# Kernel optimization log

Hardware: AMD Instinct MI355X
Metric: run time of the kernel (lower is better)

Reference implementation:

```python
import jax, jax.numpy as jnp
import numpy as np

E = 16          # num_experts
D_FULL = 1024   # full_feature_dim
DM = 128        # expert_dim
S = D_FULL // E # per-expert feature slice = 64
P = 2048        # num patches
B = 8
C = 256
W = 3           # local_window (neighbor experts)
DEPTH = 8       # cantor_depth
NEG = -1e9


def _cantor_coord(pos, max_len, depth):
    x = pos / max(1, max_len - 1)
    x = max(1e-6, min(x, 1.0 - 1e-6))
    val, factor = 0.0, 0.5
    for _ in range(depth):
        x *= 3.0
        d = int(x)
        x -= d
        if d == 2:
            val += factor
        factor *= 0.5
    return val


def _expert_routes():
    coords = np.array([_cantor_coord(i, E, DEPTH) for i in range(E)], dtype=np.float32)
    return np.stack([np.argsort(np.abs(coords - coords[i]), kind='stable')[:W] for i in range(E)]).astype(np.int32)


ROUTES = _expert_routes()  # [E, W] static routing table


def setup_inputs():
    key = jax.random.key(0)
    ks = jax.random.split(key, 8)
    h = S // 4
    lim = float(np.sqrt(6.0 / (S + DM)))  # xavier_uniform bound
    penta = jax.random.normal(ks[5], (E, 5, DM), jnp.float32) * 0.02
    penta = penta / jnp.linalg.norm(penta, axis=-1, keepdims=True)
    return {
        'tokens': jax.random.normal(ks[0], (B, P, D_FULL), jnp.float32),
        'fingerprints': jax.random.uniform(ks[1], (P,), jnp.float32),
        'alpha': jnp.ones((E,), jnp.float32),
        'gate_w1': jax.random.normal(ks[2], (E, S, h), jnp.float32) * 0.05,
        'gate_b1': jnp.zeros((E, h), jnp.float32),
        'gate_w2': jax.random.normal(ks[3], (E, h, 1), jnp.float32) * 0.05,
        'gate_b2': jnp.zeros((E, 1), jnp.float32),
        'q_w': jax.random.uniform(ks[4], (E, S, DM), jnp.float32, -lim, lim),
        'k_w': jax.random.uniform(ks[6], (E, S, DM), jnp.float32, -lim, lim),
        'v_w': jax.random.uniform(ks[7], (E, S, DM), jnp.float32, -lim, lim),
        'penta': penta,
        'fusion_w': jnp.ones((5,), jnp.float32) / 5.0,
        'temperature': jnp.float32(0.5),
    }


def _dispatch(fingerprints):
    # Fingerprint band masks, then fixed-capacity gather (static shapes for jit).
    masks = []
    for e in range(E):
        lo, hi = e / E, (e + 1) / E
        m = (fingerprints >= lo) & ((fingerprints <= hi) if e == E - 1 else (fingerprints < hi))
        masks.append(m)
    masks = jnp.stack(masks)                             # [E, P]
    order = jnp.argsort(jnp.where(masks, 0, 1), axis=1)  # stable: assigned patches first
    idx = order[:, :C]                                   # [E, C]
    valid = jnp.take_along_axis(masks, idx, axis=1)      # [E, C]
    return idx, valid


def _forward(tokens, fingerprints, alpha, gate_w1, gate_b1, gate_w2, gate_b2,
             q_w, k_w, v_w, penta, fusion_w, temperature):
    idx, valid = _dispatch(fingerprints)
    Kaff, Qaff, Vs = [], [], []
    for e in range(E):  # fixed structural loop over experts
        feats = tokens[:, idx[e], e * S:(e + 1) * S]                       # [B, C, S]
        g = jax.nn.sigmoid(jax.nn.gelu(feats @ gate_w1[e] + gate_b1[e]) @ gate_w2[e] + gate_b2[e])
        aw = jax.nn.sigmoid(alpha[e])
        feats = feats * (g * aw + (1.0 - aw))                              # gated features
        Q = feats @ q_w[e]
        K = feats @ k_w[e]
        V = feats @ v_w[e]                                                 # [B, C, DM]
        dirs = penta[e] / jnp.linalg.norm(penta[e], axis=-1, keepdims=True)  # [5, DM]
        Kaff.append(jnp.einsum('bcd,vd->vbc', K, dirs))
        Qaff.append(jnp.einsum('bcd,vd->vbc', Q, dirs))
        Vs.append(V)
    Kaff = jnp.stack(Kaff)   # [E, 5, B, C]
    Qaff = jnp.stack(Qaff)   # [E, 5, B, C]
    Vs = jnp.stack(Vs)       # [E, B, C, DM]
    wdir = jax.nn.softmax(fusion_w)
    vmask = valid.astype(jnp.float32)
    out = jnp.zeros((B, P, DM), jnp.float32)
    for e in range(E):
        nb = ROUTES[e]                                  # static [W]
        Knb, Vnb, vnb = Kaff[nb], Vs[nb], vmask[nb]     # [W,5,B,C], [W,B,C,DM], [W,C]
        scores = jnp.einsum('vbi,nvbj->vbinj', Qaff[e], Knb) / temperature
        scores = jnp.where(vnb[None, None, None, :, :] > 0, scores, NEG)
        attn = jax.nn.softmax(scores.reshape(5, B, C, W * C), axis=-1).reshape(5, B, C, W, C)
        att = jnp.einsum('vbinj,nbjd->vbid', attn, Vnb)  # per-direction attended values
        out_e = jnp.einsum('v,vbid->bid', wdir, att) * vmask[e][None, :, None]
        out = out.at[:, idx[e]].add(out_e)              # scatter back to patch positions
    return out


def reference(tokens, fingerprints, alpha, gate_w1, gate_b1, gate_w2, gate_b2,
              q_w, k_w, v_w, penta, fusion_w, temperature):
    return _forward(tokens, fingerprints, alpha, gate_w1, gate_b1, gate_w2, gate_b2,
                    q_w, k_w, v_w, penta, fusion_w, temperature)
```

## Files before the change

kernel.cpp:

```cpp
#include <hip/hip_runtime.h>
#include <cfloat>
#include <math.h>

#define E 16
#define DFULL 1024
#define DM 128
#define S 64
#define P 2048
#define B 8
#define C 256
#define W 3
#define H 16
#define RQ 16
#define NCH 16
#define LOG2E 1.4426950408889634f

typedef __attribute__((ext_vector_type(8))) short short8;
typedef __attribute__((ext_vector_type(4))) float f32x4;
#define MFMA_BF16(a, b, c) __builtin_amdgcn_mfma_f32_16x16x32_bf16((a), (b), (c), 0, 0, 0)

struct RoutesArg { int nb[E][W]; };

static void compute_routes(int r[E][W]) {
  float coords[E];
  for (int i = 0; i < E; ++i) {
    double x = (double)i / (double)(E - 1);
    if (x < 1e-06) x = 1e-06;
    if (x > 1.0 - 1e-06) x = 1.0 - 1e-06;
    double val = 0.0, factor = 0.5;
    for (int k = 0; k < 8; ++k) {
      x *= 3.0;
      int d = (int)x;
      x -= (double)d;
      if (d == 2) val += factor;
      factor *= 0.5;
    }
    coords[i] = (float)val;
  }
  for (int e = 0; e < E; ++e) {
    float de[E];
    for (int i = 0; i < E; ++i) de[i] = fabsf(coords[i] - coords[e]);
    bool used[E] = {false};
    for (int w = 0; w < W; ++w) {
      int best = -1; float bd = FLT_MAX;
      for (int i = 0; i < E; ++i)
        if (!used[i] && de[i] < bd) { bd = de[i]; best = i; }
      used[best] = true;
      r[e][w] = best;
    }
  }
}

__device__ __forceinline__ unsigned short bfhi(float x) {
  return (unsigned short)(__float_as_uint(x) >> 16);
}
__device__ __forceinline__ float bf2f(unsigned short h) {
  return __uint_as_float(((unsigned)h) << 16);
}
__device__ __forceinline__ float gelu_tanh(float x) {
  float x3 = x * x * x;
  return 0.5f * x * (1.0f + tanhf(0.7978845608028654f * (x + 0.044715f * x3)));
}
__device__ __forceinline__ float sigmoidf_(float x) {
  return 1.0f / (1.0f + __expf(-x));
}

__global__ __launch_bounds__(256) void k_setup(
    const float* __restrict__ fp, const float* __restrict__ qw,
    const float* __restrict__ kw, const float* __restrict__ penta,
    const float* __restrict__ temp, const float* __restrict__ vw,
    int* __restrict__ idx, int* __restrict__ counts,
    unsigned short* __restrict__ qkdT_h, unsigned short* __restrict__ qkdT_l,
    unsigned short* __restrict__ vwT_h, unsigned short* __restrict__ vwT_l) {
  int e = blockIdx.x, t = threadIdx.x;
  if (blockIdx.y == 1) {
    const float* vwe = vw + (size_t)e * S * DM;
    for (int u = t; u < S * DM; u += 256) {
      int d = u >> 6, s = u & 63;
      float f = vwe[(size_t)s * DM + d];
      unsigned short h = bfhi(f), l = bfhi(f - bf2f(h));
      vwT_h[(size_t)e * 8192 + u] = h;
      vwT_l[(size_t)e * 8192 + u] = l;
    }
    return;
  }
  {
    float lo = (float)e * 0.0625f, hi = (float)(e + 1) * 0.0625f;
    bool last = (e == E - 1);
    int p0 = t * 8;
    int m[8]; int ls = 0;
    #pragma unroll
    for (int k = 0; k < 8; ++k) {
      float f = fp[p0 + k];
      bool mm = (f >= lo) && (last ? (f <= hi) : (f < hi));
      m[k] = mm ? 1 : 0;
      ls += m[k];
    }
    __shared__ int sc[256];
    sc[t] = ls;
    __syncthreads();
    for (int o = 1; o < 256; o <<= 1) {
      int v = (t >= o) ? sc[t - o] : 0;
      __syncthreads();
      sc[t] += v;
      __syncthreads();
    }
    int incl = sc[t];
    int M = sc[255];
    int r = incl - ls;
    #pragma unroll
    for (int k = 0; k < 8; ++k) {
      if (m[k]) {
        if (r < C) idx[e * C + r] = p0 + k;
        r++;
      }
    }
    if (t == 0) counts[e] = (M < C) ? M : C;
  }
  __syncthreads();
  __shared__ float s_rn[5];
  if (t < 5) {
    const float* pv = penta + (e * 5 + t) * DM;
    float ss = 0.f;
    for (int d = 0; d < DM; ++d) ss += pv[d] * pv[d];
    s_rn[t] = 1.0f / sqrtf(ss);
  }
  __syncthreads();
  float invT = 1.0f / temp[0];
  int s = t & 63, cg = t >> 6;
  for (int c = cg; c < 10; c += 4) {
    int v = c % 5;
    bool isq = (c < 5);
    const float* wrow = (isq ? qw : kw) + ((size_t)e * S + s) * DM;
    const float* pv = penta + (e * 5 + v) * DM;
    float acc = 0.f;
    #pragma unroll
    for (int d4 = 0; d4 < DM / 4; ++d4) {
      float4 a = ((const float4*)wrow)[d4];
      float4 p = ((const float4*)pv)[d4];
      acc += a.x * p.x + a.y * p.y + a.z * p.z + a.w * p.w;
    }
    float val = acc * s_rn[v] * (isq ? invT : 1.0f);
    unsigned short h = bfhi(val), l = bfhi(val - bf2f(h));
    qkdT_h[(e * 16 + c) * 64 + s] = h;
    qkdT_l[(e * 16 + c) * 64 + s] = l;
  }
  for (int c = 10 + cg; c < 16; c += 4) {
    qkdT_h[(e * 16 + c) * 64 + s] = 0;
    qkdT_l[(e * 16 + c) * 64 + s] = 0;
  }
}

__global__ __launch_bounds__(256) void k_p1(
    const float* __restrict__ tokens, const float* __restrict__ alpha,
    const float* __restrict__ gw1, const float* __restrict__ gb1,
    const float* __restrict__ gw2, const float* __restrict__ gb2,
    const unsigned short* __restrict__ qkdT_h, const unsigned short* __restrict__ qkdT_l,
    const unsigned short* __restrict__ vwT_h, const unsigned short* __restrict__ vwT_l,
    const int* __restrict__ idx, const int* __restrict__ counts,
    float* __restrict__ Qa, float* __restrict__ Ka,
    unsigned short* __restrict__ Vt_h, unsigned short* __restrict__ Vt_l,
    float* __restrict__ kmx, float* __restrict__ kmn) {
  int e = blockIdx.x, b = blockIdx.y, rq = blockIdx.z;
  int t = threadIdx.x;
  int Me = counts[e];
  int r0 = rq * RQ;

  if (r0 >= Me) {
    if (t < 5) {
      kmx[((e * 5 + t) * B + b) * NCH + rq] = -FLT_MAX;
      kmn[((e * 5 + t) * B + b) * NCH + rq] = FLT_MAX;
    }
    return;
  }

  __shared__ float s_f[RQ * 65];
  __shared__ __align__(16) unsigned short s_fh[RQ * 72];
  __shared__ __align__(16) unsigned short s_fl[RQ * 72];
  __shared__ float s_gw1[S * H];
  __shared__ float s_gh[RQ * 8 * H];
  __shared__ float s_scl[RQ];
  __shared__ float s_kx[5 * RQ], s_kn[5 * RQ];
  __shared__ __align__(16) unsigned short s_vth[DM * 16];
  __shared__ __align__(16) unsigned short s_vtl[DM * 16];

  {
    int row = t >> 4, q4 = t & 15;
    int ii = r0 + row;
    int pos = (ii < Me) ? idx[e * C + ii] : idx[e * C];
    const float* trow = tokens + ((size_t)b * P + pos) * DFULL + e * S;
    float4 v4 = ((const float4*)trow)[q4];
    s_f[row * 65 + q4 * 4 + 0] = v4.x;
    s_f[row * 65 + q4 * 4 + 1] = v4.y;
    s_f[row * 65 + q4 * 4 + 2] = v4.z;
    s_f[row * 65 + q4 * 4 + 3] = v4.w;
    ((float4*)s_gw1)[t] = ((const float4*)(gw1 + (size_t)e * S * H))[t];
  }
  __syncthreads();

  if (t < 128) {
    int row = t >> 3, sq = t & 7;
    float hh[H];
    #pragma unroll
    for (int j = 0; j < H; ++j) hh[j] = 0.f;
    #pragma unroll
    for (int k = 0; k < 8; ++k) {
      int s = sq * 8 + k;
      float fs = s_f[row * 65 + s];
      const float* gr = s_gw1 + s * H;
      #pragma unroll
      for (int j = 0; j < H; ++j) hh[j] += fs * gr[j];
    }
    #pragma unroll
    for (int j = 0; j < H; ++j) s_gh[(row * 8 + sq) * H + j] = hh[j];
  }
  __syncthreads();
  if (t < RQ) {
    float z = gb2[e];
    #pragma unroll
    for (int j = 0; j < H; ++j) {
      float hj = gb1[e * H + j];
      #pragma unroll
      for (int p = 0; p < 8; ++p) hj += s_gh[(t * 8 + p) * H + j];
      z += gelu_tanh(hj) * gw2[e * H + j];
    }
    float aw = sigmoidf_(alpha[e]);
    s_scl[t] = sigmoidf_(z) * aw + (1.0f - aw);
  }
  __syncthreads();
  {
    int row = t >> 4, s0 = (t & 15) * 4;
    float sc = s_scl[row];
    #pragma unroll
    for (int k = 0; k < 4; ++k) {
      float f = s_f[row * 65 + s0 + k] * sc;
      unsigned short h = bfhi(f), l = bfhi(f - bf2f(h));
      s_fh[row * 72 + s0 + k] = h;
      s_fl[row * 72 + s0 + k] = l;
    }
  }
  __syncthreads();

  int L = t & 63, wv = t >> 6, quad = L >> 4, col = L & 15;

  {
    const unsigned short* vTh = vwT_h + (size_t)e * 8192;
    const unsigned short* vTl = vwT_l + (size_t)e * 8192;
    f32x4 va0 = {0.f, 0.f, 0.f, 0.f}, va1 = {0.f, 0.f, 0.f, 0.f};
    int d0 = wv * 32 + col, d1 = d0 + 16;
    #pragma unroll
    for (int kc = 0; kc < 2; ++kc) {
      int ko = kc * 32 + quad * 8;
      short8 ah = *(const short8*)(s_fh + col * 72 + ko);
      short8 al = *(const short8*)(s_fl + col * 72 + ko);
      short8 bh0 = *(const short8*)(vTh + d0 * 64 + ko);
      short8 bl0 = *(const short8*)(vTl + d0 * 64 + ko);
      short8 bh1 = *(const short8*)(vTh + d1 * 64 + ko);
      short8 bl1 = *(const short8*)(vTl + d1 * 64 + ko);
      va0 = MFMA_BF16(ah, bh0, va0);
      va0 = MFMA_BF16(ah, bl0, va0);
      va0 = MFMA_BF16(al, bh0, va0);
      va1 = MFMA_BF16(ah, bh1, va1);
      va1 = MFMA_BF16(ah, bl1, va1);
      va1 = MFMA_BF16(al, bh1, va1);
    }
    #pragma unroll
    for (int reg = 0; reg < 4; ++reg) {
      int row = quad * 4 + reg;
      float f0 = va0[reg];
      unsigned short h0 = bfhi(f0), l0 = bfhi(f0 - bf2f(h0));
      s_vth[d0 * 16 + row] = h0;
      s_vtl[d0 * 16 + row] = l0;
      float f1 = va1[reg];
      unsigned short h1 = bfhi(f1), l1 = bfhi(f1 - bf2f(h1));
      s_vth[d1 * 16 + row] = h1;
      s_vtl[d1 * 16 + row] = l1;
    }
  }

  if (wv == 0) {
    const unsigned short* qTh = qkdT_h + e * 16 * 64;
    const unsigned short* qTl = qkdT_l + e * 16 * 64;
    f32x4 qa = {0.f, 0.f, 0.f, 0.f};
    #pragma unroll
    for (int kc = 0; kc < 2; ++kc) {
      int ko = kc * 32 + quad * 8;
      short8 ah = *(const short8*)(s_fh + col * 72 + ko);
      short8 al = *(const short8*)(s_fl + col * 72 + ko);
      short8 bh = *(const short8*)(qTh + col * 64 + ko);
      short8 bl = *(const short8*)(qTl + col * 64 + ko);
      qa = MFMA_BF16(ah, bh, qa);
      qa = MFMA_BF16(ah, bl, qa);
      qa = MFMA_BF16(al, bh, qa);
    }
    #pragma unroll
    for (int reg = 0; reg < 4; ++reg) {
      int row = quad * 4 + reg;
      int ii = r0 + row;
      float val = qa[reg];
      if (col < 5) {
        if (ii < Me) Qa[((e * 5 + col) * B + b) * C + ii] = val;
      } else if (col < 10) {
        int v = col - 5;
        if (ii < Me) Ka[((e * 5 + v) * B + b) * C + ii] = val;
        s_kx[v * RQ + row] = (ii < Me) ? val : -FLT_MAX;
        s_kn[v * RQ + row] = (ii < Me) ? val : FLT_MAX;
      }
    }
  }
  __syncthreads();
  if (t < 5) {
    float mx = -FLT_MAX, mn = FLT_MAX;
    for (int r = 0; r < RQ; ++r) {
      mx = fmaxf(mx, s_kx[t * RQ + r]);
      mn = fminf(mn, s_kn[t * RQ + r]);
    }
    kmx[((e * 5 + t) * B + b) * NCH + rq] = mx;
    kmn[((e * 5 + t) * B + b) * NCH + rq] = mn;
  }
  {
    size_t base = ((size_t)(e * B + b) * 16 + rq) * (DM * 16);
    int off = t * 8;
    *(short8*)(Vt_h + base + off) = *(const short8*)(s_vth + off);
    *(short8*)(Vt_l + base + off) = *(const short8*)(s_vtl + off);
  }
}

__global__ __launch_bounds__(256) void k_p2v(
    const float* __restrict__ Qa, const float* __restrict__ Ka,
    const unsigned short* __restrict__ Vt_h, const unsigned short* __restrict__ Vt_l,
    const float* __restrict__ kmx, const float* __restrict__ kmn,
    const int* __restrict__ idx, const int* __restrict__ counts,
    const float* __restrict__ fusw, float* __restrict__ out, RoutesArg R) {
  int e = blockIdx.x, b = blockIdx.y, rq = blockIdx.z;
  int t = threadIdx.x;
  int Me = counts[e];
  int r0 = rq * RQ;
  if (r0 >= Me) return;

  __shared__ float s_ka[3 * 5 * C];
  __shared__ __align__(16) unsigned short s_wh[RQ * 264];
  __shared__ __align__(16) unsigned short s_wl[RQ * 264];
  __shared__ float s_lp[16 * 5 * RQ];
  __shared__ float s_KX[5], s_KN[5];
  __shared__ float s_l[5 * RQ];
  float* s_red = (float*)s_wh;

  int nbs[3] = {R.nb[e][0], R.nb[e][1], R.nb[e][2]};
  int Mns[3] = {counts[nbs[0]], counts[nbs[1]], counts[nbs[2]]};
  int row = t & 15, jq = t >> 4;
  int ii = r0 + row;

  for (int u = t; u < 3 * 5 * C; u += 256) {
    int n = u / (5 * C);
    int rem = u - n * 5 * C;
    int v = rem >> 8, j = rem & 255;
    s_ka[u] = Ka[(((size_t)nbs[n] * 5 + v) * B + b) * C + j];
  }
  if (t < 240) {
    int v = t / 48, rr = t % 48, n = rr >> 4, k = rr & 15;
    int base = ((nbs[n] * 5 + v) * B + b) * NCH + k;
    s_red[t] = kmx[base];
    s_red[240 + t] = kmn[base];
  }
  __syncthreads();
  if (t < 5) {
    float KX = -FLT_MAX, KN = FLT_MAX;
    for (int u = 0; u < 48; ++u) {
      KX = fmaxf(KX, s_red[t * 48 + u]);
      KN = fminf(KN, s_red[240 + t * 48 + u]);
    }
    s_KX[t] = KX; s_KN[t] = KN;
  }
  __syncthreads();

  float q2[5], m2[5];
  #pragma unroll
  for (int v = 0; v < 5; ++v) {
    float qv = Qa[(((size_t)e * 5 + v) * B + b) * C + ii];
    q2[v] = qv * LOG2E;
    m2[v] = ((qv > 0.f) ? qv * s_KX[v] : qv * s_KN[v]) * LOG2E;
  }

  float lp[5] = {0.f, 0.f, 0.f, 0.f, 0.f};
  for (int n = 0; n < 3; ++n) {
    int Mn = Mns[n];
    const float* kb = s_ka + n * 5 * C;
    for (int j = jq; j < Mn; j += 16) {
      #pragma unroll
      for (int v = 0; v < 5; ++v)
        lp[v] += exp2f(fmaf(q2[v], kb[v * C + j], -m2[v]));
    }
  }
  #pragma unroll
  for (int v = 0; v < 5; ++v) s_lp[(jq * 5 + v) * RQ + row] = lp[v];
  __syncthreads();
  if (t < 80) {
    int v = t >> 4, rw = t & 15;
    float l = 0.f;
    #pragma unroll
    for (int g = 0; g < 16; ++g) l += s_lp[(g * 5 + v) * RQ + rw];
    s_l[v * RQ + rw] = l;
  }
  __syncthreads();

  float fw[5];
  #pragma unroll
  for (int v = 0; v < 5; ++v) fw[v] = fusw[v];
  float fmx = fw[0];
  #pragma unroll
  for (int v = 1; v < 5; ++v) fmx = fmaxf(fmx, fw[v]);
  float fsum = 0.f;
  #pragma unroll
  for (int v = 0; v < 5; ++v) { fw[v] = __expf(fw[v] - fmx); fsum += fw[v]; }
  float c2[5];
  #pragma unroll
  for (int v = 0; v < 5; ++v) {
    float cl = (fw[v] / fsum) / s_l[v * RQ + row];
    c2[v] = __log2f(cl) - m2[v];
  }

  int L = t & 63, wv = t >> 6, quad = L >> 4, col = L & 15;
  int d0 = wv * 32 + col, d1 = d0 + 16;
  f32x4 acc0 = {0.f, 0.f, 0.f, 0.f}, acc1 = {0.f, 0.f, 0.f, 0.f};

  for (int n = 0; n < 3; ++n) {
    int ne = nbs[n], Mn = Mns[n];
    const float* kb = s_ka + n * 5 * C;
    __syncthreads();
    #pragma unroll
    for (int h8 = 0; h8 < 2; ++h8) {
      short8 wh8, wl8;
      #pragma unroll
      for (int k2 = 0; k2 < 8; ++k2) {
        int jj = jq * 16 + h8 * 8 + k2;
        float ww = 0.f;
        if (jj < Mn) {
          #pragma unroll
          for (int v = 0; v < 5; ++v)
            ww += exp2f(fmaf(q2[v], kb[v * C + jj], c2[v]));
        }
        unsigned short h = bfhi(ww), l = bfhi(ww - bf2f(h));
        wh8[k2] = (short)h;
        wl8[k2] = (short)l;
      }
      *(short8*)(s_wh + row * 264 + jq * 16 + h8 * 8) = wh8;
      *(short8*)(s_wl + row * 264 + jq * 16 + h8 * 8) = wl8;
    }
    __syncthreads();
    const unsigned short* vbh = Vt_h + (size_t)(ne * B + b) * (DM * C);
    const unsigned short* vbl = Vt_l + (size_t)(ne * B + b) * (DM * C);
    int kcN = (Mn + 31) >> 5;
    for (int kc = 0; kc < kcN; ++kc) {
      int ko = kc * 32 + quad * 8;
      short8 ah = *(const short8*)(s_wh + col * 264 + ko);
      short8 al = *(const short8*)(s_wl + col * 264 + ko);
      int jt = kc * 2 + (quad >> 1);
      size_t sb = (size_t)jt * (DM * 16) + (quad & 1) * 8;
      short8 bh0 = *(const short8*)(vbh + sb + d0 * 16);
      short8 bl0 = *(const short8*)(vbl + sb + d0 * 16);
      short8 bh1 = *(const short8*)(vbh + sb + d1 * 16);
      short8 bl1 = *(const short8*)(vbl + sb + d1 * 16);
      acc0 = MFMA_BF16(ah, bh0, acc0);
      acc0 = MFMA_BF16(ah, bl0, acc0);
      acc0 = MFMA_BF16(al, bh0, acc0);
      acc1 = MFMA_BF16(ah, bh1, acc1);
      acc1 = MFMA_BF16(ah, bl1, acc1);
      acc1 = MFMA_BF16(al, bh1, acc1);
    }
  }

  #pragma unroll
  for (int reg = 0; reg < 4; ++reg) {
    int rr = quad * 4 + reg;
    int iw = r0 + rr;
    if (iw < Me) {
      int pos = idx[e * C + iw];
      float* orow = out + ((size_t)b * P + pos) * DM;
      orow[d0] = acc0[reg];
      orow[d1] = acc1[reg];
    }
  }
}

extern "C" void kernel_launch(void* const* d_in, const int* in_sizes, int n_in,
                              void* d_out, int out_size, void* d_ws, size_t ws_size,
                              hipStream_t stream) {
  const float* tokens = (const float*)d_in[0];
  const float* fingerprints = (const float*)d_in[1];
  const float* alpha = (const float*)d_in[2];
  const float* gw1 = (const float*)d_in[3];
  const float* gb1 = (const float*)d_in[4];
  const float* gw2 = (const float*)d_in[5];
  const float* gb2 = (const float*)d_in[6];
  const float* qw = (const float*)d_in[7];
  const float* kw = (const float*)d_in[8];
  const float* vw = (const float*)d_in[9];
  const float* penta = (const float*)d_in[10];
  const float* fusw = (const float*)d_in[11];
  const float* temp = (const float*)d_in[12];
  float* out = (float*)d_out;

  float* ws = (float*)d_ws;
  float* Qa = ws;
  float* Ka = Qa + (size_t)E * 5 * B * C;
  float* kmx = Ka + (size_t)E * 5 * B * C;
  float* kmn = kmx + (size_t)E * 5 * B * NCH;
  unsigned short* qkdT_h = (unsigned short*)(kmn + (size_t)E * 5 * B * NCH);
  unsigned short* qkdT_l = qkdT_h + (size_t)E * 16 * 64;
  unsigned short* vwT_h = qkdT_l + (size_t)E * 16 * 64;
  unsigned short* vwT_l = vwT_h + (size_t)E * S * DM;
  unsigned short* Vt_h = vwT_l + (size_t)E * S * DM;
  unsigned short* Vt_l = Vt_h + (size_t)E * B * DM * C;
  int* idx = (int*)(Vt_l + (size_t)E * B * DM * C);
  int* counts = idx + (size_t)E * C;

  RoutesArg R;
  compute_routes(R.nb);

  hipMemsetAsync(d_out, 0, (size_t)out_size * sizeof(float), stream);
  k_setup<<<dim3(E, 2), dim3(256), 0, stream>>>(fingerprints, qw, kw, penta, temp, vw,
                                                idx, counts, qkdT_h, qkdT_l, vwT_h, vwT_l);
  k_p1<<<dim3(E, B, NCH), dim3(256), 0, stream>>>(tokens, alpha, gw1, gb1, gw2, gb2,
                                                  qkdT_h, qkdT_l, vwT_h, vwT_l,
                                                  idx, counts, Qa, Ka, Vt_h, Vt_l,
                                                  kmx, kmn);
  k_p2v<<<dim3(E, B, NCH), dim3(256), 0, stream>>>(Qa, Ka, Vt_h, Vt_l, kmx, kmn,
                                                   idx, counts, fusw, out, R);
}
```

Baseline: 209.0 us.

## Double threads per block, fuse output zeroing, restage neighbor keys and V layout

Launches k_p1 and k_p2v with 512 threads so each wave computes one 16-column slice of the MFMA output instead of two. It drops the separate memset and has k_p1 blocks zero the output. k_p2v now stages one neighbor's keys at a time in shared memory instead of all three, and V is stored in a layout that gives contiguous 8-element loads. k_setup transposes v_w through shared memory for coalesced reads. Together these aim at more parallelism and lower LDS use, at the cost of extra syncs per neighbor.

Result: faster. 190.7 us (-8.7%).

```diff
diff --git a/kernel.cpp b/kernel.cpp
--- a/kernel.cpp
+++ b/kernel.cpp
@@ -14,6 +14,7 @@
 #define RQ 16
 #define NCH 16
 #define LOG2E 1.4426950408889634f
+#define WST 272
 
 typedef __attribute__((ext_vector_type(8))) short short8;
 typedef __attribute__((ext_vector_type(4))) float f32x4;
@@ -73,11 +74,17 @@
     unsigned short* __restrict__ qkdT_h, unsigned short* __restrict__ qkdT_l,
     unsigned short* __restrict__ vwT_h, unsigned short* __restrict__ vwT_l) {
   int e = blockIdx.x, t = threadIdx.x;
+  __shared__ float s_tr[DM * 65];
   if (blockIdx.y == 1) {
     const float* vwe = vw + (size_t)e * S * DM;
     for (int u = t; u < S * DM; u += 256) {
+      int s = u >> 7, d = u & 127;
+      s_tr[d * 65 + s] = vwe[u];
+    }
+    __syncthreads();
+    for (int u = t; u < S * DM; u += 256) {
       int d = u >> 6, s = u & 63;
-      float f = vwe[(size_t)s * DM + d];
+      float f = s_tr[d * 65 + s];
       unsigned short h = bfhi(f), l = bfhi(f - bf2f(h));
       vwT_h[(size_t)e * 8192 + u] = h;
       vwT_l[(size_t)e * 8192 + u] = l;
@@ -151,7 +158,7 @@
   }
 }
 
-__global__ __launch_bounds__(256) void k_p1(
+__global__ __launch_bounds__(512, 8) void k_p1(
     const float* __restrict__ tokens, const float* __restrict__ alpha,
     const float* __restrict__ gw1, const float* __restrict__ gb1,
     const float* __restrict__ gw2, const float* __restrict__ gb2,
@@ -160,12 +167,21 @@
     const int* __restrict__ idx, const int* __restrict__ counts,
     float* __restrict__ Qa, float* __restrict__ Ka,
     unsigned short* __restrict__ Vt_h, unsigned short* __restrict__ Vt_l,
-    float* __restrict__ kmx, float* __restrict__ kmn) {
+    float* __restrict__ kmx, float* __restrict__ kmn,
+    float* __restrict__ out) {
   int e = blockIdx.x, b = blockIdx.y, rq = blockIdx.z;
   int t = threadIdx.x;
+
+  {
+    int blk = (e * B + b) * NCH + rq;
+    if (t < 256) {
+      float4 z4 = {0.f, 0.f, 0.f, 0.f};
+      ((float4*)out)[(size_t)blk * 256 + t] = z4;
+    }
+  }
+
   int Me = counts[e];
   int r0 = rq * RQ;
-
   if (r0 >= Me) {
     if (t < 5) {
       kmx[((e * 5 + t) * B + b) * NCH + rq] = -FLT_MAX;
@@ -184,7 +200,7 @@
   __shared__ __align__(16) unsigned short s_vth[DM * 16];
   __shared__ __align__(16) unsigned short s_vtl[DM * 16];
 
-  {
+  if (t < 256) {
     int row = t >> 4, q4 = t & 15;
     int ii = r0 + row;
     int pos = (ii < Me) ? idx[e * C + ii] : idx[e * C];
@@ -228,7 +244,7 @@
     s_scl[t] = sigmoidf_(z) * aw + (1.0f - aw);
   }
   __syncthreads();
-  {
+  if (t < 256) {
     int row = t >> 4, s0 = (t & 15) * 4;
     float sc = s_scl[row];
     #pragma unroll
@@ -246,35 +262,26 @@
   {
     const unsigned short* vTh = vwT_h + (size_t)e * 8192;
     const unsigned short* vTl = vwT_l + (size_t)e * 8192;
-    f32x4 va0 = {0.f, 0.f, 0.f, 0.f}, va1 = {0.f, 0.f, 0.f, 0.f};
-    int d0 = wv * 32 + col, d1 = d0 + 16;
+    f32x4 va = {0.f, 0.f, 0.f, 0.f};
+    int d0 = wv * 16 + col;
     #pragma unroll
     for (int kc = 0; kc < 2; ++kc) {
       int ko = kc * 32 + quad * 8;
       short8 ah = *(const short8*)(s_fh + col * 72 + ko);
       short8 al = *(const short8*)(s_fl + col * 72 + ko);
-      short8 bh0 = *(const short8*)(vTh + d0 * 64 + ko);
-      short8 bl0 = *(const short8*)(vTl + d0 * 64 + ko);
-      short8 bh1 = *(const short8*)(vTh + d1 * 64 + ko);
-      short8 bl1 = *(const short8*)(vTl + d1 * 64 + ko);
-      va0 = MFMA_BF16(ah, bh0, va0);
-      va0 = MFMA_BF16(ah, bl0, va0);
-      va0 = MFMA_BF16(al, bh0, va0);
-      va1 = MFMA_BF16(ah, bh1, va1);
-      va1 = MFMA_BF16(ah, bl1, va1);
-      va1 = MFMA_BF16(al, bh1, va1);
+      short8 bh = *(const short8*)(vTh + d0 * 64 + ko);
+      short8 bl = *(const short8*)(vTl + d0 * 64 + ko);
+      va = MFMA_BF16(ah, bh, va);
+      va = MFMA_BF16(ah, bl, va);
+      va = MFMA_BF16(al, bh, va);
     }
     #pragma unroll
     for (int reg = 0; reg < 4; ++reg) {
       int row = quad * 4 + reg;
-      float f0 = va0[reg];
+      float f0 = va[reg];
       unsigned short h0 = bfhi(f0), l0 = bfhi(f0 - bf2f(h0));
       s_vth[d0 * 16 + row] = h0;
       s_vtl[d0 * 16 + row] = l0;
-      float f1 = va1[reg];
-      unsigned short h1 = bfhi(f1), l1 = bfhi(f1 - bf2f(h1));
-      s_vth[d1 * 16 + row] = h1;
-      s_vtl[d1 * 16 + row] = l1;
     }
   }
 
@@ -318,15 +325,17 @@
     kmx[((e * 5 + t) * B + b) * NCH + rq] = mx;
     kmn[((e * 5 + t) * B + b) * NCH + rq] = mn;
   }
-  {
-    size_t base = ((size_t)(e * B + b) * 16 + rq) * (DM * 16);
-    int off = t * 8;
-    *(short8*)(Vt_h + base + off) = *(const short8*)(s_vth + off);
-    *(short8*)(Vt_l + base + off) = *(const short8*)(s_vtl + off);
-  }
-}
-
-__global__ __launch_bounds__(256) void k_p2v(
+  if (t < 256) {
+    size_t base = (size_t)(e * B + b) * (DM * C);
+    int jsl = t >> 7, d = t & 127;
+    size_t dst = base + ((size_t)(rq * 2 + jsl) * DM + d) * 8;
+    int src = d * 16 + jsl * 8;
+    *(short8*)(Vt_h + dst) = *(const short8*)(s_vth + src);
+    *(short8*)(Vt_l + dst) = *(const short8*)(s_vtl + src);
+  }
+}
+
+__global__ __launch_bounds__(512, 8) void k_p2v(
     const float* __restrict__ Qa, const float* __restrict__ Ka,
     const unsigned short* __restrict__ Vt_h, const unsigned short* __restrict__ Vt_l,
     const float* __restrict__ kmx, const float* __restrict__ kmn,
@@ -338,10 +347,10 @@
   int r0 = rq * RQ;
   if (r0 >= Me) return;
 
-  __shared__ float s_ka[3 * 5 * C];
-  __shared__ __align__(16) unsigned short s_wh[RQ * 264];
-  __shared__ __align__(16) unsigned short s_wl[RQ * 264];
-  __shared__ float s_lp[16 * 5 * RQ];
+  __shared__ float s_ka[5 * C];
+  __shared__ __align__(16) unsigned short s_wh[RQ * WST];
+  __shared__ __align__(16) unsigned short s_wl[RQ * WST];
+  __shared__ float s_lp[32 * 5 * RQ];
   __shared__ float s_KX[5], s_KN[5];
   __shared__ float s_l[5 * RQ];
   float* s_red = (float*)s_wh;
@@ -351,12 +360,6 @@
   int row = t & 15, jq = t >> 4;
   int ii = r0 + row;
 
-  for (int u = t; u < 3 * 5 * C; u += 256) {
-    int n = u / (5 * C);
-    int rem = u - n * 5 * C;
-    int v = rem >> 8, j = rem & 255;
-    s_ka[u] = Ka[(((size_t)nbs[n] * 5 + v) * B + b) * C + j];
-  }
   if (t < 240) {
     int v = t / 48, rr = t % 48, n = rr >> 4, k = rr & 15;
     int base = ((nbs[n] * 5 + v) * B + b) * NCH + k;
@@ -384,12 +387,18 @@
 
   float lp[5] = {0.f, 0.f, 0.f, 0.f, 0.f};
   for (int n = 0; n < 3; ++n) {
+    __syncthreads();
+    if (t < 320) {
+      int v = t >> 6, off = t & 63;
+      ((float4*)s_ka)[v * 64 + off] =
+          ((const float4*)(Ka + (((size_t)nbs[n] * 5 + v) * B + b) * C))[off];
+    }
+    __syncthreads();
     int Mn = Mns[n];
-    const float* kb = s_ka + n * 5 * C;
-    for (int j = jq; j < Mn; j += 16) {
+    for (int j = jq; j < Mn; j += 32) {
       #pragma unroll
       for (int v = 0; v < 5; ++v)
-        lp[v] += exp2f(fmaf(q2[v], kb[v * C + j], -m2[v]));
+        lp[v] += exp2f(fmaf(q2[v], s_ka[v * C + j], -m2[v]));
     }
   }
   #pragma unroll
@@ -399,7 +408,7 @@
     int v = t >> 4, rw = t & 15;
     float l = 0.f;
     #pragma unroll
-    for (int g = 0; g < 16; ++g) l += s_lp[(g * 5 + v) * RQ + rw];
+    for (int g = 0; g < 32; ++g) l += s_lp[(g * 5 + v) * RQ + rw];
     s_l[v * RQ + rw] = l;
   }
   __syncthreads();
@@ -421,31 +430,35 @@
   }
 
   int L = t & 63, wv = t >> 6, quad = L >> 4, col = L & 15;
-  int d0 = wv * 32 + col, d1 = d0 + 16;
-  f32x4 acc0 = {0.f, 0.f, 0.f, 0.f}, acc1 = {0.f, 0.f, 0.f, 0.f};
+  int d0 = wv * 16 + col;
+  f32x4 acc = {0.f, 0.f, 0.f, 0.f};
 
   for (int n = 0; n < 3; ++n) {
     int ne = nbs[n], Mn = Mns[n];
-    const float* kb = s_ka + n * 5 * C;
-    __syncthreads();
-    #pragma unroll
-    for (int h8 = 0; h8 < 2; ++h8) {
+    __syncthreads();
+    if (t < 320) {
+      int v = t >> 6, off = t & 63;
+      ((float4*)s_ka)[v * 64 + off] =
+          ((const float4*)(Ka + (((size_t)ne * 5 + v) * B + b) * C))[off];
+    }
+    __syncthreads();
+    {
       short8 wh8, wl8;
       #pragma unroll
       for (int k2 = 0; k2 < 8; ++k2) {
-        int jj = jq * 16 + h8 * 8 + k2;
+        int jj = jq * 8 + k2;
         float ww = 0.f;
         if (jj < Mn) {
           #pragma unroll
           for (int v = 0; v < 5; ++v)
-            ww += exp2f(fmaf(q2[v], kb[v * C + jj], c2[v]));
+            ww += exp2f(fmaf(q2[v], s_ka[v * C + jj], c2[v]));
         }
         unsigned short h = bfhi(ww), l = bfhi(ww - bf2f(h));
         wh8[k2] = (short)h;
         wl8[k2] = (short)l;
       }
-      *(short8*)(s_wh + row * 264 + jq * 16 + h8 * 8) = wh8;
-      *(short8*)(s_wl + row * 264 + jq * 16 + h8 * 8) = wl8;
+      *(short8*)(s_wh + row * WST + jq * 8) = wh8;
+      *(short8*)(s_wl + row * WST + jq * 8) = wl8;
     }
     __syncthreads();
     const unsigned short* vbh = Vt_h + (size_t)(ne * B + b) * (DM * C);
@@ -453,20 +466,14 @@
     int kcN = (Mn + 31) >> 5;
     for (int kc = 0; kc < kcN; ++kc) {
       int ko = kc * 32 + quad * 8;
-      short8 ah = *(const short8*)(s_wh + col * 264 + ko);
-      short8 al = *(const short8*)(s_wl + col * 264 + ko);
-      int jt = kc * 2 + (quad >> 1);
-      size_t sb = (size_t)jt * (DM * 16) + (quad & 1) * 8;
-      short8 bh0 = *(const short8*)(vbh + sb + d0 * 16);
-      short8 bl0 = *(const short8*)(vbl + sb + d0 * 16);
-      short8 bh1 = *(const short8*)(vbh + sb + d1 * 16);
-      short8 bl1 = *(const short8*)(vbl + sb + d1 * 16);
-      acc0 = MFMA_BF16(ah, bh0, acc0);
-      acc0 = MFMA_BF16(ah, bl0, acc0);
-      acc0 = MFMA_BF16(al, bh0, acc0);
-      acc1 = MFMA_BF16(ah, bh1, acc1);
-      acc1 = MFMA_BF16(ah, bl1, acc1);
-      acc1 = MFMA_BF16(al, bh1, acc1);
+      short8 ah = *(const short8*)(s_wh + col * WST + ko);
+      short8 al = *(const short8*)(s_wl + col * WST + ko);
+      size_t sb = ((size_t)(kc * 4 + quad) * DM + d0) * 8;
+      short8 bh = *(const short8*)(vbh + sb);
+      short8 bl = *(const short8*)(vbl + sb);
+      acc = MFMA_BF16(ah, bh, acc);
+      acc = MFMA_BF16(ah, bl, acc);
+      acc = MFMA_BF16(al, bh, acc);
     }
   }
 
@@ -476,9 +483,7 @@
     int iw = r0 + rr;
     if (iw < Me) {
       int pos = idx[e * C + iw];
-      float* orow = out + ((size_t)b * P + pos) * DM;
-      orow[d0] = acc0[reg];
-      orow[d1] = acc1[reg];
+      out[((size_t)b * P + pos) * DM + d0] = acc[reg];
     }
   }
 }
@@ -518,13 +523,12 @@
   RoutesArg R;
   compute_routes(R.nb);
 
-  hipMemsetAsync(d_out, 0, (size_t)out_size * sizeof(float), stream);
   k_setup<<<dim3(E, 2), dim3(256), 0, stream>>>(fingerprints, qw, kw, penta, temp, vw,
                                                 idx, counts, qkdT_h, qkdT_l, vwT_h, vwT_l);
-  k_p1<<<dim3(E, B, NCH), dim3(256), 0, stream>>>(tokens, alpha, gw1, gb1, gw2, gb2,
+  k_p1<<<dim3(E, B, NCH), dim3(512), 0, stream>>>(tokens, alpha, gw1, gb1, gw2, gb2,
                                                   qkdT_h, qkdT_l, vwT_h, vwT_l,
                                                   idx, counts, Qa, Ka, Vt_h, Vt_l,
-                                                  kmx, kmn);
-  k_p2v<<<dim3(E, B, NCH), dim3(256), 0, stream>>>(Qa, Ka, Vt_h, Vt_l, kmx, kmn,
+                                                  kmx, kmn, out);
+  k_p2v<<<dim3(E, B, NCH), dim3(512), 0, stream>>>(Qa, Ka, Vt_h, Vt_l, kmx, kmn,
                                                    idx, counts, fusw, out, R);
 }
```
